# Optimization experiments

Measured on AMD Instinct MI355X. Metric: run time of the kernel, lower is better.

Reference implementation:

```python
import jax, jax.numpy as jnp
import numpy as np

B, N, CIN, COUT, MAXN, NF, MID = 8, 512, 64, 64, 16, 32, 16
M1 = [3, 32, 32, 1]
M2 = [CIN * COUT, 512, MID]
MR = [CIN * MID, 512, COUT]
BN_EPS = 1e-3  # keras BatchNormalization default epsilon


def mish(v):
    return v * jnp.tanh(jax.nn.softplus(v))


def bn(v, g, b):
    # training-mode batch norm over the row axis (keras BN in learning phase)
    mu = jnp.mean(v, axis=0, keepdims=True)
    var = jnp.var(v, axis=0, keepdims=True)
    return g * (v - mu) * jax.lax.rsqrt(var + BN_EPS) + b


def _mlp(v, layers):
    for W, b, g, be in layers:
        v = bn(mish(v @ W + b), g, be)
    return v


def setup_inputs() -> dict:
    key = jax.random.key(0)
    ks = jax.random.split(key, 16)
    inp = {
        'x': jax.random.normal(ks[0], (B, N, CIN), jnp.float32),
        'xyz': jax.random.normal(ks[1], (B, N, 3), jnp.float32),
        'framepoints': jax.random.normal(ks[2], (NF, 3), jnp.float32),
        'fpw': jax.random.normal(ks[3], (NF, CIN, COUT), jnp.float32) * 0.05,
    }
    ki = 4
    for name, dims in (('m1', M1), ('m2', M2), ('mr', MR)):
        for i in range(len(dims) - 1):
            inp[f'{name}_w{i}'] = jax.random.normal(ks[ki], (dims[i], dims[i + 1]), jnp.float32) / np.float32(np.sqrt(dims[i]))
            inp[f'{name}_b{i}'] = jnp.zeros((dims[i + 1],), jnp.float32)
            inp[f'{name}_g{i}'] = jnp.ones((dims[i + 1],), jnp.float32)
            inp[f'{name}_be{i}'] = jnp.zeros((dims[i + 1],), jnp.float32)
            ki += 1
    return inp


def reference(x, xyz, framepoints, fpw,
              m1_w0, m1_b0, m1_g0, m1_be0,
              m1_w1, m1_b1, m1_g1, m1_be1,
              m1_w2, m1_b2, m1_g2, m1_be2,
              m2_w0, m2_b0, m2_g0, m2_be0,
              m2_w1, m2_b1, m2_g1, m2_be1,
              mr_w0, mr_b0, mr_g0, mr_be0,
              mr_w1, mr_b1, mr_g1, mr_be1):
    Bc, Nc, cin = x.shape
    nf = framepoints.shape[0]
    cout = fpw.shape[2]
    mid = m2_w1.shape[1]

    # pairwise squared distances on FEATURES (as in the original), gram form
    sq = jnp.sum(x * x, axis=-1)  # [B,N]
    d = sq[:, :, None] + sq[:, None, :] - 2.0 * jnp.einsum('bnc,bmc->bnm', x, x)
    _, idx = jax.lax.top_k(-d, MAXN)  # [B,N,maxn] nearest (self first)

    bidx = jnp.arange(Bc)[:, None, None]
    xyz_sl = xyz[bidx, idx]  # [B,N,maxn,3]
    fur = x[bidx, idx]       # [B,N,maxn,cin]

    xyz_sl = xyz_sl.reshape(-1, MAXN, 3)
    rel = (xyz_sl - xyz_sl[:, :1, :]).reshape(-1, 3)  # [B*N*maxn, 3]

    # deterministic random rotation of frame points about the y axis
    ang = jax.random.uniform(jax.random.key(42), ()) * 2.0 * jnp.pi
    c = jnp.cos(ang); s = jnp.sin(ang)
    z = jnp.zeros_like(c); o = jnp.ones_like(c)
    R = jnp.stack([jnp.stack([c, z, s]), jnp.stack([z, o, z]), jnp.stack([-s, z, c])])
    fp = framepoints @ R  # [nf,3]

    sl = jnp.concatenate([rel, fp], axis=0)              # [M+nf, 3]
    diff = (sl[:, None, :] - fp[None, :, :]).reshape(-1, 3)  # [(M+nf)*nf, 3]

    h = _mlp(diff, [(m1_w0, m1_b0, m1_g0, m1_be0),
                    (m1_w1, m1_b1, m1_g1, m1_be1),
                    (m1_w2, m1_b2, m1_g2, m1_be2)])      # [(M+nf)*nf, 1]

    w = _mlp(fpw.reshape(nf, -1), [(m2_w0, m2_b0, m2_g0, m2_be0),
                                   (m2_w1, m2_b1, m2_g1, m2_be1)])  # [nf, mid]

    agg = jnp.sum(h.reshape(-1, nf, 1) * w[None], axis=1)  # [M+nf, mid]
    wmain = agg[:-nf].reshape(-1, MAXN, mid)               # [B*N, maxn, mid]

    f = jnp.einsum('kmc,kmd->kcd', fur.reshape(-1, MAXN, cin), wmain)
    f = f.reshape(-1, cin * mid)
    f = _mlp(f, [(mr_w0, mr_b0, mr_g0, mr_be0),
                 (mr_w1, mr_b1, mr_g1, mr_be1)])           # [B*N, cout]
    return f.reshape(Bc, Nc, cout)
```

## Files before the change

### kernel.cpp

```cpp
#include <hip/hip_runtime.h>
#include <math.h>

#define BB    8
#define NN    512
#define CIN   64
#define MAXN  16
#define NF    32
#define MID   16
#define BN_   4096
#define MSL   65536
#define MTOT  65568
#define RROWS 2098176
#define P2STR 40

typedef unsigned short ushort_t;
typedef __attribute__((ext_vector_type(8))) short bf16x8;
typedef __attribute__((ext_vector_type(4))) float f32x4;

__device__ __forceinline__ float mishf(float x){
  float t  = __expf(x);
  float u  = 1.0f + t;
  float u2 = u * u;
  float r  = x * (u2 - 1.0f) * __builtin_amdgcn_rcpf(u2 + 1.0f);
  return (x > 15.0f) ? x : r;
}

__device__ __forceinline__ ushort_t f2bf(float f){
  unsigned u = __float_as_uint(f);
  unsigned r = (u + 0x7FFFu + ((u >> 16) & 1u)) >> 16;
  return (ushort_t)r;
}

__device__ __forceinline__ unsigned cvt_pk_bf16(float lo, float hi){
  unsigned r;
  asm("v_cvt_pk_bf16_f32 %0, %1, %2" : "=v"(r) : "v"(lo), "v"(hi));
  return r;
}

__device__ __forceinline__ unsigned rotl32(unsigned v, unsigned s){
  return (v << s) | (v >> (32u - s));
}

__device__ __forceinline__ float jax_uniform42(){
  unsigned ks[3];
  ks[0] = 0u; ks[1] = 42u; ks[2] = 0x1BD11BDAu ^ 0u ^ 42u;
  const unsigned rot[8] = {13u,15u,26u,6u,17u,29u,16u,24u};
  unsigned x0 = ks[0];
  unsigned x1 = ks[1];
  #pragma unroll
  for (int blk = 0; blk < 5; ++blk){
    #pragma unroll
    for (int r = 0; r < 4; ++r){
      x0 += x1;
      x1 = rotl32(x1, rot[(blk & 1) * 4 + r]);
      x1 ^= x0;
    }
    x0 += ks[(blk + 1) % 3];
    x1 += ks[(blk + 2) % 3] + (unsigned)(blk + 1);
  }
  unsigned w = x0 ^ x1;
  return __uint_as_float((w >> 9) | 0x3f800000u) - 1.0f;
}

__global__ __launch_bounds__(256) void k_sq(const float* __restrict__ x, double* __restrict__ sqd){
  int r = blockIdx.x * 256 + threadIdx.x;
  const float4* p = (const float4*)(x + (size_t)r * 64);
  double a0 = 0.0, a1 = 0.0, a2 = 0.0, a3 = 0.0;
  #pragma unroll
  for (int k = 0; k < 16; k += 4){
    float4 v0 = p[k], v1 = p[k+1], v2 = p[k+2], v3 = p[k+3];
    a0 += (double)v0.x*v0.x + (double)v0.y*v0.y + (double)v0.z*v0.z + (double)v0.w*v0.w;
    a1 += (double)v1.x*v1.x + (double)v1.y*v1.y + (double)v1.z*v1.z + (double)v1.w*v1.w;
    a2 += (double)v2.x*v2.x + (double)v2.y*v2.y + (double)v2.z*v2.z + (double)v2.w*v2.w;
    a3 += (double)v3.x*v3.x + (double)v3.y*v3.y + (double)v3.z*v3.z + (double)v3.w*v3.w;
  }
  sqd[r] = (a0 + a1) + (a2 + a3);
}

__global__ __launch_bounds__(256) void k_topk(const float* __restrict__ x, const double* __restrict__ sqd,
                                              int* __restrict__ idxp){
  __shared__ float ct[128 * 65];
  __shared__ float xnl[4][64];
  int tid  = threadIdx.x;
  int lane = tid & 63;
  int wid  = tid >> 6;
  int g = blockIdx.x * 4 + wid;
  int b = g >> 9;
  const float* xb = x + (size_t)b * (NN * CIN);
  {
    int w = tid >> 6, c = tid & 63;
    int nq = (blockIdx.x * 4 + w) & 511;
    xnl[w][c] = xb[nq * 64 + c];
  }
  double sqn = sqd[g];

  double dst[8];
  #pragma unroll 1
  for (int tile = 0; tile < 4; ++tile){
    __syncthreads();
    #pragma unroll
    for (int u = 0; u < 8; ++u){
      int idx = u * 256 + tid;
      int row = idx >> 4, q = idx & 15;
      float4 v = *(const float4*)&xb[(size_t)(tile * 128 + row) * 64 + q * 4];
      float* d = &ct[row * 65 + q * 4];
      d[0] = v.x; d[1] = v.y; d[2] = v.z; d[3] = v.w;
    }
    __syncthreads();
    double a[2][4];
    #pragma unroll
    for (int s = 0; s < 2; ++s)
      #pragma unroll
      for (int i = 0; i < 4; ++i) a[s][i] = 0.0;
    #pragma unroll
    for (int k = 0; k < 16; ++k){
      float4 qv = *(const float4*)&xnl[wid][k * 4];
      double q0 = (double)qv.x, q1 = (double)qv.y, q2 = (double)qv.z, q3 = (double)qv.w;
      #pragma unroll
      for (int s = 0; s < 2; ++s){
        const float* rp = &ct[(lane + 64 * s) * 65 + k * 4];
        a[s][0] += q0 * (double)rp[0];
        a[s][1] += q1 * (double)rp[1];
        a[s][2] += q2 * (double)rp[2];
        a[s][3] += q3 * (double)rp[3];
      }
    }
    #pragma unroll
    for (int s = 0; s < 2; ++s){
      int m = tile * 128 + 64 * s + lane;
      dst[tile * 2 + s] = sqn + sqd[(b << 9) + m] - 2.0 * ((a[s][0] + a[s][1]) + (a[s][2] + a[s][3]));
    }
  }

  for (int it = 0; it < 16; ++it){
    double bd = 1.0e300; int bi = 0x7FFFFFFF;
    #pragma unroll
    for (int j = 0; j < 8; ++j){
      int m = ((j >> 1) << 7) + ((j & 1) << 6) + lane;
      if (dst[j] < bd){ bd = dst[j]; bi = m; }
    }
    #pragma unroll
    for (int off = 1; off < 64; off <<= 1){
      double od = __shfl_xor(bd, off);
      int    oi = __shfl_xor(bi, off);
      if (od < bd || (od == bd && oi < bi)){ bd = od; bi = oi; }
    }
    if (lane == 0) idxp[g * 16 + it] = bi;
    if (lane == (bi & 63)){
      int slot = ((bi >> 7) << 1) | ((bi >> 6) & 1);
      #pragma unroll
      for (int j = 0; j < 8; ++j) if (j == slot) dst[j] = 1.0e300;
    }
  }
}

__global__ __launch_bounds__(256) void k_prep(const float* __restrict__ xyz,
                                              const float* __restrict__ fpts,
                                              const int* __restrict__ idxp,
                                              const float* __restrict__ w0, const float* __restrict__ b0,
                                              float* __restrict__ sib, float* __restrict__ fjt){
  __shared__ float w0l[96], b0l[32];
  int tid = threadIdx.x;
  if (tid < 96) w0l[tid] = w0[tid];
  else if (tid < 128) b0l[tid - 96] = b0[tid - 96];
  __syncthreads();
  int i = blockIdx.x * 256 + tid;
  if (i >= MTOT) return;
  float vx, vy, vz;
  if (i < MSL){
    int bn = i >> 4, m = i & 15, b = bn >> 9;
    int i0 = idxp[bn * 16];
    int im = idxp[bn * 16 + m];
    const float* xz = xyz + (size_t)b * (NN * 3);
    vx = xz[im * 3 + 0] - xz[i0 * 3 + 0];
    vy = xz[im * 3 + 1] - xz[i0 * 3 + 1];
    vz = xz[im * 3 + 2] - xz[i0 * 3 + 2];
  } else {
    int j = i - MSL;
    float u   = jax_uniform42();
    float ang = (u * 2.0f) * 3.14159274f;
    float c = cosf(ang), s = sinf(ang);
    float fx = fpts[j * 3 + 0], fy = fpts[j * 3 + 1], fz = fpts[j * 3 + 2];
    vx = fx * c - fz * s;
    vy = fy;
    vz = fx * s + fz * c;
  }
  float si[32];
  #pragma unroll
  for (int c = 0; c < 32; ++c)
    si[c] = vx * w0l[c] + vy * w0l[32 + c] + vz * w0l[64 + c];
  float* dst = sib + (size_t)i * 32;
  #pragma unroll
  for (int cq = 0; cq < 8; ++cq){
    float4 o = make_float4(si[cq*4+0] + b0l[cq*4+0], si[cq*4+1] + b0l[cq*4+1],
                           si[cq*4+2] + b0l[cq*4+2], si[cq*4+3] + b0l[cq*4+3]);
    *(float4*)&dst[cq*4] = o;
  }
  if (i >= MSL){
    int j = i - MSL;
    #pragma unroll
    for (int c = 0; c < 32; ++c) fjt[c * 32 + j] = si[c];
  }
}

__global__ __launch_bounds__(256) void k_m1_p1(const float* __restrict__ sib, const float* __restrict__ fjt,
                                               float* __restrict__ s0g, float* __restrict__ q0g,
                                               ushort_t* __restrict__ a0g){
  __shared__ float fjlt[32 * 33];
  __shared__ float red[16][32], redq[16][32];
  int tid = threadIdx.x;
  for (int t = tid; t < 1024; t += 256) fjlt[(t & 31) * 33 + (t >> 5)] = fjt[t];
  __syncthreads();
  int c2 = (tid & 15) * 2, s = tid >> 4;
  float as0 = 0.0f, aq0 = 0.0f, as1 = 0.0f, aq1 = 0.0f;
  int base = blockIdx.x * 1024;
  #pragma unroll 4
  for (int t = 0; t < 64; ++t){
    int r = base + t * 16 + s;
    int i = r >> 5, j = r & 31;
    float2 v = *(const float2*)&sib[(size_t)i * 32 + c2];
    float2 f = *(const float2*)&fjlt[j * 33 + c2];
    float m0 = mishf(v.x - f.x);
    float m1 = mishf(v.y - f.y);
    as0 += m0; aq0 += m0 * m0;
    as1 += m1; aq1 += m1 * m1;
    if (a0g) *(unsigned*)&a0g[(size_t)r * 32 + c2] = cvt_pk_bf16(m0, m1);
  }
  red[s][c2] = as0;  red[s][c2 + 1] = as1;
  redq[s][c2] = aq0; redq[s][c2 + 1] = aq1;
  __syncthreads();
  if (tid < 32){
    float ts = 0.0f, tq = 0.0f;
    #pragma unroll
    for (int ss = 0; ss < 16; ++ss){ ts += red[ss][tid]; tq += redq[ss][tid]; }
    int bank = (blockIdx.x & 15) * 32 + tid;
    atomicAdd(&s0g[bank], ts);
    atomicAdd(&q0g[bank], tq);
  }
}

__global__ __launch_bounds__(256) void k_m1_setup(const float* __restrict__ w1g, const float* __restrict__ b1g,
                                                  const float* __restrict__ g0, const float* __restrict__ be0,
                                                  const float* __restrict__ s0g, const float* __restrict__ q0g,
                                                  float* __restrict__ biasXg, ushort_t* __restrict__ wtsb){
  __shared__ float A0l[32], C0l[32];
  int tid = threadIdx.x;
  if (tid < 32){
    float s = 0.0f, q = 0.0f;
    #pragma unroll
    for (int b = 0; b < 16; ++b){ s += s0g[b * 32 + tid]; q += q0g[b * 32 + tid]; }
    const float invR = 1.0f / (float)RROWS;
    float mu = s * invR, var = q * invR - mu * mu;
    float A = g0[tid] * rsqrtf(var + 1e-3f);
    A0l[tid] = A; C0l[tid] = be0[tid] - mu * A;
  }
  __syncthreads();
  if (tid < 32){
    float acc = b1g[tid];
    #pragma unroll
    for (int k = 0; k < 32; ++k) acc += C0l[k] * w1g[k * 32 + tid];
    biasXg[tid] = acc;
  }
  for (int t = tid; t < 1024; t += 256){
    int k = t >> 5, c = t & 31;
    wtsb[c * 32 + k] = f2bf(w1g[t] * A0l[k]);
  }
}

__global__ __launch_bounds__(256, 8) void k_m1_p2f(const ushort_t* __restrict__ a0g,
                                                   const ushort_t* __restrict__ wtsb,
                                                   const float* __restrict__ biasXg,
                                                   float* __restrict__ s1g, float* __restrict__ q1g,
                                                   ushort_t* __restrict__ a1b){
  __shared__ float satm[32], qatm[32];
  int tid = threadIdx.x;
  if (tid < 32){ satm[tid] = 0.0f; qatm[tid] = 0.0f; }
  __syncthreads();
  int lane = tid & 63, w = tid >> 6;
  int ln15 = lane & 15, quad = lane >> 4;
  bf16x8 bfr0 = *(const bf16x8*)&wtsb[ln15 * 32 + quad * 8];
  bf16x8 bfr1 = *(const bf16x8*)&wtsb[(16 + ln15) * 32 + quad * 8];
  f32x4 zero = {0.0f, 0.0f, 0.0f, 0.0f};
  f32x4 acc[4][2];
  size_t rowt = (size_t)blockIdx.x * 256;
  #pragma unroll
  for (int i2 = 0; i2 < 4; ++i2){
    int row = (w * 4 + i2) * 16 + ln15;
    bf16x8 af = *(const bf16x8*)&a0g[(rowt + row) * 32 + quad * 8];
    acc[i2][0] = __builtin_amdgcn_mfma_f32_16x16x32_bf16(af, bfr0, zero, 0, 0, 0);
    acc[i2][1] = __builtin_amdgcn_mfma_f32_16x16x32_bf16(af, bfr1, zero, 0, 0, 0);
  }
  float cs[2] = {0.0f, 0.0f}, cq2[2] = {0.0f, 0.0f};
  size_t rowbase = rowt + w * 64 + quad * 4;
  #pragma unroll
  for (int nt = 0; nt < 2; ++nt){
    int col = nt * 16 + ln15;
    float bx = biasXg[col];
    size_t colbase = (size_t)col * RROWS;
    #pragma unroll
    for (int i2 = 0; i2 < 4; ++i2){
      f32x4 a = acc[i2][nt];
      float m0 = mishf(a[0] + bx);
      float m1 = mishf(a[1] + bx);
      float m2 = mishf(a[2] + bx);
      float m3 = mishf(a[3] + bx);
      cs[nt]  += m0 + m1 + m2 + m3;
      cq2[nt] += m0*m0 + m1*m1 + m2*m2 + m3*m3;
      uint2 pk;
      pk.x = cvt_pk_bf16(m0, m1);
      pk.y = cvt_pk_bf16(m2, m3);
      *(uint2*)&a1b[colbase + rowbase + (size_t)i2 * 16] = pk;
    }
  }
  #pragma unroll
  for (int nt = 0; nt < 2; ++nt){
    float v = cs[nt], u = cq2[nt];
    v += __shfl_xor(v, 16); u += __shfl_xor(u, 16);
    v += __shfl_xor(v, 32); u += __shfl_xor(u, 32);
    if (lane < 16){
      atomicAdd(&satm[nt * 16 + ln15], v);
      atomicAdd(&qatm[nt * 16 + ln15], u);
    }
  }
  __syncthreads();
  if (tid < 32){
    int bank = (blockIdx.x & 15) * 32 + tid;
    atomicAdd(&s1g[bank], satm[tid]);
    atomicAdd(&q1g[bank], qatm[tid]);
  }
}

__global__ __launch_bounds__(256, 6) void k_m1_p2(const float* __restrict__ sib, const float* __restrict__ fjt,
                                               const float* __restrict__ w1g, const float* __restrict__ b1g,
                                               const float* __restrict__ g0, const float* __restrict__ be0,
                                               const float* __restrict__ s0g, const float* __restrict__ q0g,
                                               float* __restrict__ s1g, float* __restrict__ q1g,
                                               ushort_t* __restrict__ a1b){
  __shared__ __align__(16) ushort_t a0s[256 * P2STR];
  __shared__ __align__(16) float uni[1024];
  __shared__ float A0l[32], C0l[32], biasX[32], satm[32], qatm[32];
  ushort_t* wts = (ushort_t*)uni;
  int tid = threadIdx.x;
  for (int t = tid; t < 1024; t += 256) uni[t] = fjt[t];
  if (tid < 32){
    float s = 0.0f, q = 0.0f;
    #pragma unroll
    for (int b = 0; b < 16; ++b){ s += s0g[b * 32 + tid]; q += q0g[b * 32 + tid]; }
    const float invR = 1.0f / (float)RROWS;
    float mu = s * invR, var = q * invR - mu * mu;
    float A = g0[tid] * rsqrtf(var + 1e-3f);
    A0l[tid] = A; C0l[tid] = be0[tid] - mu * A;
    satm[tid] = 0.0f; qatm[tid] = 0.0f;
  }
  __syncthreads();
  {
    int r = blockIdx.x * 256 + tid;
    int i = r >> 5, j = r & 31;
    const float* sr = sib + (size_t)i * 32;
    ushort_t* dst = &a0s[tid * P2STR];
    #pragma unroll
    for (int cq = 0; cq < 4; ++cq){
      float4 sa = *(const float4*)&sr[cq * 8];
      float4 sb = *(const float4*)&sr[cq * 8 + 4];
      float m0 = mishf(sa.x - uni[(cq*8+0)*32 + j]);
      float m1 = mishf(sa.y - uni[(cq*8+1)*32 + j]);
      float m2 = mishf(sa.z - uni[(cq*8+2)*32 + j]);
      float m3 = mishf(sa.w - uni[(cq*8+3)*32 + j]);
      float m4 = mishf(sb.x - uni[(cq*8+4)*32 + j]);
      float m5 = mishf(sb.y - uni[(cq*8+5)*32 + j]);
      float m6 = mishf(sb.z - uni[(cq*8+6)*32 + j]);
      float m7 = mishf(sb.w - uni[(cq*8+7)*32 + j]);
      uint4 pk;
      pk.x = cvt_pk_bf16(m0, m1);
      pk.y = cvt_pk_bf16(m2, m3);
      pk.z = cvt_pk_bf16(m4, m5);
      pk.w = cvt_pk_bf16(m6, m7);
      *(uint4*)&dst[cq * 8] = pk;
    }
  }
  if (tid < 32){
    float acc = b1g[tid];
    #pragma unroll
    for (int k = 0; k < 32; ++k) acc += C0l[k] * w1g[k * 32 + tid];
    biasX[tid] = acc;
  }
  __syncthreads();
  for (int t = tid; t < 1024; t += 256){
    int k = t >> 5, c = t & 31;
    wts[c * P2STR + k] = f2bf(w1g[t] * A0l[k]);
  }
  __syncthreads();
  int lane = tid & 63, w = tid >> 6;
  int ln15 = lane & 15, quad = lane >> 4;
  f32x4 zero = {0.0f, 0.0f, 0.0f, 0.0f};
  bf16x8 bfr0 = *(bf16x8*)&wts[(ln15) * P2STR + quad * 8];
  bf16x8 bfr1 = *(bf16x8*)&wts[(16 + ln15) * P2STR + quad * 8];
  f32x4 acc[4][2];
  #pragma unroll
  for (int i2 = 0; i2 < 4; ++i2){
    int row = (w * 4 + i2) * 16 + ln15;
    bf16x8 af = *(bf16x8*)&a0s[row * P2STR + quad * 8];
    acc[i2][0] = __builtin_amdgcn_mfma_f32_16x16x32_bf16(af, bfr0, zero, 0, 0, 0);
    acc[i2][1] = __builtin_amdgcn_mfma_f32_16x16x32_bf16(af, bfr1, zero, 0, 0, 0);
  }
  float cs[2] = {0.0f, 0.0f}, cq2[2] = {0.0f, 0.0f};
  size_t rowbase = (size_t)blockIdx.x * 256 + w * 64 + quad * 4;
  #pragma unroll
  for (int nt = 0; nt < 2; ++nt){
    int col = nt * 16 + ln15;
    float bx = biasX[col];
    size_t colbase = (size_t)col * RROWS;
    #pragma unroll
    for (int i2 = 0; i2 < 4; ++i2){
      f32x4 a = acc[i2][nt];
      float m0 = mishf(a[0] + bx);
      float m1 = mishf(a[1] + bx);
      float m2 = mishf(a[2] + bx);
      float m3 = mishf(a[3] + bx);
      cs[nt]  += m0 + m1 + m2 + m3;
      cq2[nt] += m0*m0 + m1*m1 + m2*m2 + m3*m3;
      if (a1b){
        uint2 pk;
        pk.x = cvt_pk_bf16(m0, m1);
        pk.y = cvt_pk_bf16(m2, m3);
        *(uint2*)&a1b[colbase + rowbase + (size_t)i2 * 16] = pk;
      }
    }
  }
  #pragma unroll
  for (int nt = 0; nt < 2; ++nt){
    float v = cs[nt], u = cq2[nt];
    v += __shfl_xor(v, 16); u += __shfl_xor(u, 16);
    v += __shfl_xor(v, 32); u += __shfl_xor(u, 32);
    if (lane < 16){
      atomicAdd(&satm[nt * 16 + ln15], v);
      atomicAdd(&qatm[nt * 16 + ln15], u);
    }
  }
  __syncthreads();
  if (tid < 32){
    int bank = (blockIdx.x & 15) * 32 + tid;
    atomicAdd(&s1g[bank], satm[tid]);
    atomicAdd(&q1g[bank], qatm[tid]);
  }
}

__global__ __launch_bounds__(256) void k_m1_p3s(const ushort_t* __restrict__ a1b,
                                                const float* __restrict__ w2g, const float* __restrict__ b2g,
                                                const float* __restrict__ g1, const float* __restrict__ be1,
                                                const float* __restrict__ s1g, const float* __restrict__ q1g,
                                                float* __restrict__ act2, float* __restrict__ s2g, float* __restrict__ q2g){
  __shared__ float vvl[32], C1l[32], cb2l[1], r2s[4], r2q[4];
  int tid = threadIdx.x;
  if (tid < 32){
    float s = 0.0f, q = 0.0f;
    #pragma unroll
    for (int b = 0; b < 16; ++b){ s += s1g[b * 32 + tid]; q += q1g[b * 32 + tid]; }
    const float invR = 1.0f / (float)RROWS;
    float mu = s * invR, var = q * invR - mu * mu;
    float A = g1[tid] * rsqrtf(var + 1e-3f);
    C1l[tid] = be1[tid] - mu * A;
    vvl[tid] = A * w2g[tid];
  }
  __syncthreads();
  if (tid == 0){
    float a = b2g[0];
    #pragma unroll
    for (int k = 0; k < 32; ++k) a += C1l[k] * w2g[k];
    cb2l[0] = a;
  }
  __syncthreads();
  size_t r0 = (size_t)blockIdx.x * 2048 + (size_t)tid * 8;
  float ss = 0.0f, qq = 0.0f;
  if (r0 < (size_t)RROWS){
    float pre[8];
    #pragma unroll
    for (int j = 0; j < 8; ++j) pre[j] = 0.0f;
    #pragma unroll 8
    for (int c = 0; c < 32; ++c){
      uint4 u = *(const uint4*)&a1b[(size_t)c * RROWS + r0];
      float vv = vvl[c];
      pre[0] += __uint_as_float(u.x << 16) * vv;
      pre[1] += __uint_as_float(u.x & 0xFFFF0000u) * vv;
      pre[2] += __uint_as_float(u.y << 16) * vv;
      pre[3] += __uint_as_float(u.y & 0xFFFF0000u) * vv;
      pre[4] += __uint_as_float(u.z << 16) * vv;
      pre[5] += __uint_as_float(u.z & 0xFFFF0000u) * vv;
      pre[6] += __uint_as_float(u.w << 16) * vv;
      pre[7] += __uint_as_float(u.w & 0xFFFF0000u) * vv;
    }
    float cb2 = cb2l[0];
    float a2[8];
    #pragma unroll
    for (int j = 0; j < 8; ++j){
      a2[j] = mishf(pre[j] + cb2);
      ss += a2[j]; qq += a2[j] * a2[j];
    }
    *(float4*)&act2[r0]     = make_float4(a2[0], a2[1], a2[2], a2[3]);
    *(float4*)&act2[r0 + 4] = make_float4(a2[4], a2[5], a2[6], a2[7]);
  }
  #pragma unroll
  for (int off = 1; off < 64; off <<= 1){ ss += __shfl_xor(ss, off); qq += __shfl_xor(qq, off); }
  int lane = tid & 63, wid = tid >> 6;
  if (lane == 0){ r2s[wid] = ss; r2q[wid] = qq; }
  __syncthreads();
  if (tid == 0){
    atomicAdd(&s2g[blockIdx.x & 15], r2s[0] + r2s[1] + r2s[2] + r2s[3]);
    atomicAdd(&q2g[blockIdx.x & 15], r2q[0] + r2q[1] + r2q[2] + r2q[3]);
  }
}

__global__ __launch_bounds__(256, 3) void k_m1_p3f(const float* __restrict__ sib, const float* __restrict__ fjt,
                                               const float* __restrict__ w1g, const float* __restrict__ b1g,
                                               const float* __restrict__ g0, const float* __restrict__ be0,
                                               const float* __restrict__ g1, const float* __restrict__ be1,
                                               const float* __restrict__ w2g, const float* __restrict__ b2g,
                                               const float* __restrict__ s0g, const float* __restrict__ q0g,
                                               const float* __restrict__ s1g, const float* __restrict__ q1g,
                                               float* __restrict__ act2, float* __restrict__ s2g, float* __restrict__ q2g){
  __shared__ float fjl[1024];
  __shared__ float w1s[1024];
  __shared__ float A0l[32], C0l[32], A1l[32], C1l[32], biasX[32], vvl[32];
  __shared__ float a0t[32 * 256];
  __shared__ float cb2l[1];
  __shared__ float r2s[4], r2q[4];
  int tid = threadIdx.x;
  const float invR = 1.0f / (float)RROWS;
  for (int t = tid; t < 1024; t += 256) fjl[t] = fjt[t];
  if (tid < 32){
    float s = 0.0f, q = 0.0f;
    #pragma unroll
    for (int b = 0; b < 16; ++b){ s += s0g[b * 32 + tid]; q += q0g[b * 32 + tid]; }
    float mu = s * invR, var = q * invR - mu * mu;
    float A = g0[tid] * rsqrtf(var + 1e-3f);
    A0l[tid] = A; C0l[tid] = be0[tid] - mu * A;
  } else if (tid < 64){
    int c = tid - 32;
    float s = 0.0f, q = 0.0f;
    #pragma unroll
    for (int b = 0; b < 16; ++b){ s += s1g[b * 32 + c]; q += q1g[b * 32 + c]; }
    float mu = s * invR, var = q * invR - mu * mu;
    float A = g1[c] * rsqrtf(var + 1e-3f);
    A1l[c] = A; C1l[c] = be1[c] - mu * A;
  }
  __syncthreads();
  for (int t = tid; t < 1024; t += 256) w1s[t] = w1g[t] * A0l[t >> 5];
  if (tid < 32){
    float acc = b1g[tid];
    #pragma unroll
    for (int k = 0; k < 32; ++k) acc += C0l[k] * w1g[k * 32 + tid];
    biasX[tid] = acc;
  } else if (tid < 96 && tid >= 64){
    int c = tid - 64;
    vvl[c] = A1l[c] * w2g[c];
  } else if (tid == 96){
    float acc = b2g[0];
    #pragma unroll
    for (int k = 0; k < 32; ++k) acc += C1l[k] * w2g[k];
    cb2l[0] = acc;
  }
  {
    int r = blockIdx.x * 256 + tid;
    int i = r >> 5, j = r & 31;
    const float* sr = sib + (size_t)i * 32;
    #pragma unroll
    for (int cq = 0; cq < 8; ++cq){
      float4 sv = *(const float4*)&sr[cq * 4];
      a0t[(cq*4+0)*256 + tid] = mishf(sv.x - fjl[(cq*4+0)*32 + j]);
      a0t[(cq*4+1)*256 + tid] = mishf(sv.y - fjl[(cq*4+1)*32 + j]);
      a0t[(cq*4+2)*256 + tid] = mishf(sv.z - fjl[(cq*4+2)*32 + j]);
      a0t[(cq*4+3)*256 + tid] = mishf(sv.w - fjl[(cq*4+3)*32 + j]);
    }
  }
  __syncthreads();
  int cg = tid & 7, rg = tid >> 3;
  float acc[8][4];
  #pragma unroll
  for (int i2 = 0; i2 < 8; ++i2)
    #pragma unroll
    for (int j2 = 0; j2 < 4; ++j2) acc[i2][j2] = 0.0f;
  #pragma unroll 4
  for (int k = 0; k < 32; ++k){
    float4 w  = *(const float4*)&w1s[k * 32 + cg * 4];
    float4 aA = *(const float4*)&a0t[k * 256 + rg * 8];
    float4 aB = *(const float4*)&a0t[k * 256 + rg * 8 + 4];
    float ar[8] = {aA.x, aA.y, aA.z, aA.w, aB.x, aB.y, aB.z, aB.w};
    float wc[4] = {w.x, w.y, w.z, w.w};
    #pragma unroll
    for (int i2 = 0; i2 < 8; ++i2)
      #pragma unroll
      for (int j2 = 0; j2 < 4; ++j2) acc[i2][j2] += ar[i2] * wc[j2];
  }
  float cb2 = cb2l[0];
  float ss = 0.0f, qq = 0.0f;
  #pragma unroll
  for (int rr = 0; rr < 8; ++rr){
    float part = 0.0f;
    #pragma unroll
    for (int cc = 0; cc < 4; ++cc){
      float m = mishf(acc[rr][cc] + biasX[cg * 4 + cc]);
      part += m * vvl[cg * 4 + cc];
    }
    part += __shfl_xor(part, 1);
    part += __shfl_xor(part, 2);
    part += __shfl_xor(part, 4);
    float a2 = mishf(part + cb2);
    if (cg == 0){
      act2[(size_t)blockIdx.x * 256 + rg * 8 + rr] = a2;
      ss += a2; qq += a2 * a2;
    }
  }
  #pragma unroll
  for (int off = 1; off < 64; off <<= 1){ ss += __shfl_xor(ss, off); qq += __shfl_xor(qq, off); }
  int lane = tid & 63, wid = tid >> 6;
  if (lane == 0){ r2s[wid] = ss; r2q[wid] = qq; }
  __syncthreads();
  if (tid == 0){
    atomicAdd(&s2g[blockIdx.x & 15], r2s[0] + r2s[1] + r2s[2] + r2s[3]);
    atomicAdd(&q2g[blockIdx.x & 15], r2q[0] + r2q[1] + r2q[2] + r2q[3]);
  }
}

__global__ __launch_bounds__(512) void k_wmlp1(const float* __restrict__ fpw, const float* __restrict__ W0,
                                               float* __restrict__ wact0){
  int f = blockIdx.x, kc = blockIdx.y, c = threadIdx.x;
  const float* row = fpw + (size_t)f * 4096 + kc * 512;
  const float* wp  = W0 + (size_t)(kc * 512) * 512 + c;
  float acc = 0.0f;
  #pragma unroll 8
  for (int k = 0; k < 512; ++k) acc += row[k] * wp[(size_t)k * 512];
  atomicAdd(&wact0[f * 512 + c], acc);
}

__global__ __launch_bounds__(512) void k_wmlp2(const float* __restrict__ wact0, const float* __restrict__ b0,
                                               const float* __restrict__ W1,
                                               const float* __restrict__ b1,
                                               const float* __restrict__ g0, const float* __restrict__ be0,
                                               const float* __restrict__ g1, const float* __restrict__ be1,
                                               float* __restrict__ wfin){
  __shared__ float wl[32 * 512];
  __shared__ float o2l[512], A1l[16], C1l[16];
  int t = threadIdx.x;
  {
    float b0t = b0[t];
    float v[32]; float sum = 0.0f, sq = 0.0f;
    #pragma unroll
    for (int r = 0; r < 32; ++r){
      v[r] = mishf(wact0[r * 512 + t] + b0t);
      sum += v[r]; sq += v[r] * v[r];
    }
    float mu  = sum * (1.0f / 32.0f);
    float var = sq * (1.0f / 32.0f) - mu * mu;
    float A = g0[t] * rsqrtf(var + 1e-3f);
    float C = be0[t] - mu * A;
    #pragma unroll
    for (int r = 0; r < 32; ++r) wl[r * 512 + t] = v[r] * A + C;
  }
  __syncthreads();
  {
    int r = t >> 4, c2 = t & 15;
    float pre = b1[c2];
    for (int k = 0; k < 512; ++k) pre += wl[r * 512 + k] * W1[k * 16 + c2];
    o2l[t] = mishf(pre);
  }
  __syncthreads();
  if (t < 16){
    float sum = 0.0f, sq = 0.0f;
    #pragma unroll
    for (int r = 0; r < 32; ++r){ float v = o2l[r * 16 + t]; sum += v; sq += v * v; }
    float mu  = sum * (1.0f / 32.0f);
    float var = sq * (1.0f / 32.0f) - mu * mu;
    float A = g1[t] * rsqrtf(var + 1e-3f);
    A1l[t] = A; C1l[t] = be1[t] - mu * A;
  }
  __syncthreads();
  wfin[t] = o2l[t] * A1l[t & 15] + C1l[t & 15];
}

__global__ __launch_bounds__(256) void k_agg(const float* __restrict__ act2, const float* __restrict__ wfin,
                                             const float* __restrict__ x, const int* __restrict__ idxp,
                                             const float* __restrict__ s2, const float* __restrict__ q2,
                                             const float* __restrict__ g2, const float* __restrict__ be2,
                                             ushort_t* __restrict__ fb16){
  __shared__ float hl[512], wfl[512], wm[256], furl[1024], AC[2];
  int t = threadIdx.x;
  int k = blockIdx.x;
  if (t == 0){
    const float invR = 1.0f / (float)RROWS;
    float ssum = 0.0f, qsum = 0.0f;
    #pragma unroll
    for (int b = 0; b < 16; ++b){ ssum += s2[b]; qsum += q2[b]; }
    float mu  = ssum * invR;
    float var = qsum * invR - mu * mu;
    float A = g2[0] * rsqrtf(var + 1e-3f);
    AC[0] = A; AC[1] = be2[0] - mu * A;
  }
  wfl[t] = wfin[t]; wfl[t + 256] = wfin[t + 256];
  __syncthreads();
  float A2 = AC[0], C2 = AC[1];
  hl[t]       = act2[(size_t)k * 512 + t]       * A2 + C2;
  hl[t + 256] = act2[(size_t)k * 512 + 256 + t] * A2 + C2;
  __syncthreads();
  {
    int m = t >> 4, d = t & 15;
    float acc = 0.0f;
    #pragma unroll
    for (int j = 0; j < 32; ++j) acc += hl[m * 32 + j] * wfl[j * 16 + d];
    wm[t] = acc;
  }
  int b = k >> 9;
  const float* xb = x + (size_t)b * (NN * CIN);
  {
    int c = t & 63;
    #pragma unroll
    for (int it = 0; it < 4; ++it){
      int m = it * 4 + (t >> 6);
      int im = idxp[k * 16 + m];
      furl[m * 64 + c] = xb[im * 64 + c];
    }
  }
  __syncthreads();
  {
    int d = t & 15, c0 = t >> 4;
    #pragma unroll
    for (int q = 0; q < 4; ++q){
      int c = c0 + 16 * q;
      float acc = 0.0f;
      #pragma unroll
      for (int m = 0; m < 16; ++m) acc += furl[m * 64 + c] * wm[m * 16 + d];
      fb16[(size_t)k * 1024 + t + 256 * q] = f2bf(acc);
    }
  }
}

__global__ __launch_bounds__(256) void k_w2bf(const float* __restrict__ W, ushort_t* __restrict__ Wb){
  int id = blockIdx.x * 256 + threadIdx.x;
  int n  = id >> 7;
  int k8 = (id & 127) * 8;
  float v[8];
  #pragma unroll
  for (int j = 0; j < 8; ++j) v[j] = W[(size_t)(k8 + j) * 512 + n];
  uint4 p;
  p.x = cvt_pk_bf16(v[0], v[1]);
  p.y = cvt_pk_bf16(v[2], v[3]);
  p.z = cvt_pk_bf16(v[4], v[5]);
  p.w = cvt_pk_bf16(v[6], v[7]);
  *(uint4*)&Wb[(size_t)n * 1024 + k8] = p;
}

__global__ __launch_bounds__(256, 8) void k_mr1(const ushort_t* __restrict__ F16, const ushort_t* __restrict__ Wb,
                                             const float* __restrict__ bias, float* __restrict__ out,
                                             float* __restrict__ s3, float* __restrict__ q3){
  __shared__ float csum[64], csq[64];
  int tid = threadIdx.x;
  int m0 = blockIdx.y * 64, n0 = blockIdx.x * 64;
  int lane = tid & 63, w = tid >> 6;
  int ln15 = lane & 15, quad = lane >> 4;
  if (tid < 64){ csum[tid] = 0.0f; csq[tid] = 0.0f; }
  __syncthreads();
  f32x4 acc[4];
  #pragma unroll
  for (int n = 0; n < 4; ++n){ acc[n][0] = 0.0f; acc[n][1] = 0.0f; acc[n][2] = 0.0f; acc[n][3] = 0.0f; }
  const ushort_t* Arow = &F16[(size_t)(m0 + w * 16 + ln15) * 1024 + quad * 8];
  const ushort_t* B0 = &Wb[(size_t)(n0 +  0 + ln15) * 1024 + quad * 8];
  const ushort_t* B1 = &Wb[(size_t)(n0 + 16 + ln15) * 1024 + quad * 8];
  const ushort_t* B2 = &Wb[(size_t)(n0 + 32 + ln15) * 1024 + quad * 8];
  const ushort_t* B3 = &Wb[(size_t)(n0 + 48 + ln15) * 1024 + quad * 8];
  #pragma unroll 4
  for (int k0 = 0; k0 < 1024; k0 += 32){
    bf16x8 af = *(const bf16x8*)&Arow[k0];
    bf16x8 b0 = *(const bf16x8*)&B0[k0];
    bf16x8 b1 = *(const bf16x8*)&B1[k0];
    bf16x8 b2 = *(const bf16x8*)&B2[k0];
    bf16x8 b3 = *(const bf16x8*)&B3[k0];
    acc[0] = __builtin_amdgcn_mfma_f32_16x16x32_bf16(af, b0, acc[0], 0, 0, 0);
    acc[1] = __builtin_amdgcn_mfma_f32_16x16x32_bf16(af, b1, acc[1], 0, 0, 0);
    acc[2] = __builtin_amdgcn_mfma_f32_16x16x32_bf16(af, b2, acc[2], 0, 0, 0);
    acc[3] = __builtin_amdgcn_mfma_f32_16x16x32_bf16(af, b3, acc[3], 0, 0, 0);
  }
  #pragma unroll
  for (int n = 0; n < 4; ++n){
    int col = n0 + n * 16 + ln15;
    float bv = bias[col];
    f32x4 a = acc[n];
    float s = 0.0f, q = 0.0f;
    #pragma unroll
    for (int r = 0; r < 4; ++r){
      float v = mishf(a[r] + bv);
      int row = m0 + w * 16 + quad * 4 + r;
      out[(size_t)row * 512 + col] = v;
      s += v; q += v * v;
    }
    s += __shfl_xor(s, 16); q += __shfl_xor(q, 16);
    s += __shfl_xor(s, 32); q += __shfl_xor(q, 32);
    if (quad == 0){
      atomicAdd(&csum[n * 16 + ln15], s);
      atomicAdd(&csq[n * 16 + ln15], q);
    }
  }
  __syncthreads();
  if (tid < 64){
    atomicAdd(&s3[n0 + tid], csum[tid]);
    atomicAdd(&q3[n0 + tid], csq[tid]);
  }
}

__global__ __launch_bounds__(256) void k_mr2(const float* __restrict__ Ain, const float* __restrict__ W,
                                             const float* __restrict__ bias,
                                             const float* __restrict__ s3, const float* __restrict__ q3,
                                             const float* __restrict__ g0, const float* __restrict__ be0,
                                             float* __restrict__ out, float* __restrict__ s4, float* __restrict__ q4){
  __shared__ float As2[16][68];
  __shared__ float Bs2[16][68];
  __shared__ float A3l[512], C3l[512];
  __shared__ float csum[64], csq[64];
  int tid = threadIdx.x;
  for (int kk = tid; kk < 512; kk += 256){
    const float invR = 1.0f / 4096.0f;
    float mu  = s3[kk] * invR;
    float var = q3[kk] * invR - mu * mu;
    float A = g0[kk] * rsqrtf(var + 1e-3f);
    A3l[kk] = A; C3l[kk] = be0[kk] - mu * A;
  }
  if (tid < 64){ csum[tid] = 0.0f; csq[tid] = 0.0f; }
  __syncthreads();
  int m0 = blockIdx.x * 64;
  int tx = tid & 15, ty = tid >> 4;
  float acc[4][4];
  #pragma unroll
  for (int i = 0; i < 4; ++i)
    #pragma unroll
    for (int j = 0; j < 4; ++j) acc[i][j] = 0.0f;
  int lmm = tid >> 2, lkq = (tid & 3) * 4;
  int lkk = tid >> 4, lnq = (tid & 15) * 4;
  float4 av = *(const float4*)&Ain[(size_t)(m0 + lmm) * 512 + lkq];
  float4 bv = *(const float4*)&W[(size_t)lkk * 64 + lnq];
  for (int k0 = 0; k0 < 512; k0 += 16){
    As2[lkq + 0][lmm] = av.x * A3l[k0 + lkq + 0] + C3l[k0 + lkq + 0];
    As2[lkq + 1][lmm] = av.y * A3l[k0 + lkq + 1] + C3l[k0 + lkq + 1];
    As2[lkq + 2][lmm] = av.z * A3l[k0 + lkq + 2] + C3l[k0 + lkq + 2];
    As2[lkq + 3][lmm] = av.w * A3l[k0 + lkq + 3] + C3l[k0 + lkq + 3];
    *(float4*)&Bs2[lkk][lnq] = bv;
    __syncthreads();
    if (k0 + 16 < 512){
      av = *(const float4*)&Ain[(size_t)(m0 + lmm) * 512 + (k0 + 16) + lkq];
      bv = *(const float4*)&W[(size_t)((k0 + 16) + lkk) * 64 + lnq];
    }
    #pragma unroll
    for (int kk = 0; kk < 16; ++kk){
      float4 a4 = *(const float4*)&As2[kk][ty * 4];
      float4 b4 = *(const float4*)&Bs2[kk][tx * 4];
      float a[4] = {a4.x, a4.y, a4.z, a4.w};
      float bb[4] = {b4.x, b4.y, b4.z, b4.w};
      #pragma unroll
      for (int i = 0; i < 4; ++i)
        #pragma unroll
        for (int j = 0; j < 4; ++j) acc[i][j] += a[i] * bb[j];
    }
    __syncthreads();
  }
  float4 bq = *(const float4*)&bias[tx * 4];
  float bvs[4] = {bq.x, bq.y, bq.z, bq.w};
  float cs[4] = {0,0,0,0}, cq[4] = {0,0,0,0};
  #pragma unroll
  for (int i = 0; i < 4; ++i){
    float v[4];
    #pragma unroll
    for (int j = 0; j < 4; ++j){
      v[j] = mishf(acc[i][j] + bvs[j]);
      cs[j] += v[j]; cq[j] += v[j] * v[j];
    }
    float4 o = make_float4(v[0], v[1], v[2], v[3]);
    *(float4*)&out[(size_t)(m0 + ty * 4 + i) * 64 + tx * 4] = o;
  }
  #pragma unroll
  for (int j = 0; j < 4; ++j){
    float v = cs[j], w = cq[j];
    v += __shfl_xor(v, 16); w += __shfl_xor(w, 16);
    v += __shfl_xor(v, 32); w += __shfl_xor(w, 32);
    if ((tid & 63) < 16){
      atomicAdd(&csum[tx * 4 + j], v);
      atomicAdd(&csq[tx * 4 + j], w);
    }
  }
  __syncthreads();
  if (tid < 64){
    atomicAdd(&s4[tid], csum[tid]);
    atomicAdd(&q4[tid], csq[tid]);
  }
}

__global__ __launch_bounds__(256) void k_out(const float* __restrict__ pre,
                                             const float* __restrict__ s4, const float* __restrict__ q4,
                                             const float* __restrict__ g1, const float* __restrict__ be1,
                                             float* __restrict__ outp){
  int e = blockIdx.x * 256 + threadIdx.x;
  int c = e & 63;
  const float invR = 1.0f / 4096.0f;
  float mu  = s4[c] * invR;
  float var = q4[c] * invR - mu * mu;
  float A = g1[c] * rsqrtf(var + 1e-3f);
  outp[e] = pre[e] * A + (be1[c] - mu * A);
}

extern "C" void kernel_launch(void* const* d_in, const int* in_sizes, int n_in,
                              void* d_out, int out_size, void* d_ws, size_t ws_size,
                              hipStream_t stream){
  (void)in_sizes; (void)n_in; (void)out_size;
  const float* x    = (const float*)d_in[0];
  const float* xyz  = (const float*)d_in[1];
  const float* fpts = (const float*)d_in[2];
  const float* fpw  = (const float*)d_in[3];
  const float* m1w0 = (const float*)d_in[4];
  const float* m1b0 = (const float*)d_in[5];
  const float* m1g0 = (const float*)d_in[6];
  const float* m1be0= (const float*)d_in[7];
  const float* m1w1 = (const float*)d_in[8];
  const float* m1b1 = (const float*)d_in[9];
  const float* m1g1 = (const float*)d_in[10];
  const float* m1be1= (const float*)d_in[11];
  const float* m1w2 = (const float*)d_in[12];
  const float* m1b2 = (const float*)d_in[13];
  const float* m1g2 = (const float*)d_in[14];
  const float* m1be2= (const float*)d_in[15];
  const float* m2w0 = (const float*)d_in[16];
  const float* m2b0 = (const float*)d_in[17];
  const float* m2g0 = (const float*)d_in[18];
  const float* m2be0= (const float*)d_in[19];
  const float* m2w1 = (const float*)d_in[20];
  const float* m2b1 = (const float*)d_in[21];
  const float* m2g1 = (const float*)d_in[22];
  const float* m2be1= (const float*)d_in[23];
  const float* mrw0 = (const float*)d_in[24];
  const float* mrb0 = (const float*)d_in[25];
  const float* mrg0 = (const float*)d_in[26];
  const float* mrbe0= (const float*)d_in[27];
  const float* mrw1 = (const float*)d_in[28];
  const float* mrb1 = (const float*)d_in[29];
  const float* mrg1 = (const float*)d_in[30];
  const float* mrbe1= (const float*)d_in[31];

  float* wsf = (float*)d_ws;
  float* s0 = wsf + 0;     float* q0 = wsf + 512;
  float* s1 = wsf + 1024;  float* q1 = wsf + 1536;
  float* s2 = wsf + 2048;  float* q2 = wsf + 2064;
  float* s3 = wsf + 2080;  float* q3 = wsf + 2592;
  float* s4 = wsf + 3104;  float* q4 = wsf + 3168;
  int*   idxp = (int*)(wsf + 4096);
  double* sqd = (double*)(wsf + 69632);
  float* biasXg = wsf + 77824;
  ushort_t* wtsb = (ushort_t*)(wsf + 77856);
  float* wact0= wsf + 332032;
  float* wfin = wsf + 348416;
  float* act2 = wsf + 348928;
  float* fbuf = wsf + 2447104;
  float* sib  = fbuf;
  float* fjt  = fbuf + 2098176;
  ushort_t* fb16 = (ushort_t*)fbuf;
  ushort_t* wb16 = (ushort_t*)(fbuf + 2099200);
  float* mact = wsf + 6641408;
  float* mact2= wsf + 8738560;

  size_t need1 = 9000704ULL * 4 + (size_t)RROWS * 32 * 2;
  size_t need2 = need1 + (size_t)RROWS * 32 * 2;
  bool fast = (ws_size >= need1);
  bool t2   = (ws_size >= need2);
  ushort_t* a1b = fast ? (ushort_t*)(wsf + 9000704) : nullptr;
  ushort_t* a0g = t2   ? (ushort_t*)(wsf + 9000704 + 33570816) : nullptr;

  hipMemsetAsync(d_ws, 0, 4096 * sizeof(float), stream);
  hipMemsetAsync(wact0, 0, 16384 * sizeof(float), stream);

  k_w2bf<<<256, 256, 0, stream>>>(mrw0, wb16);
  k_sq<<<16, 256, 0, stream>>>(x, sqd);
  k_topk<<<1024, 256, 0, stream>>>(x, sqd, idxp);
  k_prep<<<257, 256, 0, stream>>>(xyz, fpts, idxp, m1w0, m1b0, sib, fjt);
  k_m1_p1<<<2049, 256, 0, stream>>>(sib, fjt, s0, q0, a0g);
  if (t2){
    k_m1_setup<<<1, 256, 0, stream>>>(m1w1, m1b1, m1g0, m1be0, s0, q0, biasXg, wtsb);
    k_m1_p2f<<<8196, 256, 0, stream>>>(a0g, wtsb, biasXg, s1, q1, a1b);
  } else {
    k_m1_p2<<<8196, 256, 0, stream>>>(sib, fjt, m1w1, m1b1, m1g0, m1be0, s0, q0, s1, q1, a1b);
  }
  if (fast){
    k_m1_p3s<<<1025, 256, 0, stream>>>(a1b, m1w2, m1b2, m1g1, m1be1, s1, q1, act2, s2, q2);
  } else {
    k_m1_p3f<<<8196, 256, 0, stream>>>(sib, fjt, m1w1, m1b1, m1g0, m1be0, m1g1, m1be1,
                                       m1w2, m1b2, s0, q0, s1, q1, act2, s2, q2);
  }
  k_wmlp1<<<dim3(32, 8), 512, 0, stream>>>(fpw, m2w0, wact0);
  k_wmlp2<<<1, 512, 0, stream>>>(wact0, m2b0, m2w1, m2b1, m2g0, m2be0, m2g1, m2be1, wfin);
  k_agg<<<4096, 256, 0, stream>>>(act2, wfin, x, idxp, s2, q2, m1g2, m1be2, fb16);
  k_mr1<<<dim3(8, 64), 256, 0, stream>>>(fb16, wb16, mrb0, mact, s3, q3);
  k_mr2<<<64, 256, 0, stream>>>(mact, mrw1, mrb1, s3, q3, mrg0, mrbe0, mact2, s4, q4);
  k_out<<<1024, 256, 0, stream>>>(mact2, s4, q4, mrg1, mrbe1, (float*)d_out);
}
```

Baseline: 446.3 us.

## Reuse one row-major bf16 buffer for layer-1 and layer-2 MLP activations in place

The second MLP layer now writes its bf16 activations back into the same row-major buffer that held its input, instead of into a separate column-major buffer. The third-layer kernel is rewritten to read 32 contiguous bf16 values per row and reduce them. This halves the workspace needed for the fast path, so the MFMA path runs whenever the single buffer fits. In-place writes are 2-byte scattered stores per lane, which may coalesce worse than the previous packed column stores, and they rely on each block only overwriting rows it has already read.

```diff
diff --git a/kernel.cpp b/kernel.cpp
--- a/kernel.cpp
+++ b/kernel.cpp
@@ -267,11 +267,10 @@
   }
 }
 
-__global__ __launch_bounds__(256, 8) void k_m1_p2f(const ushort_t* __restrict__ a0g,
+__global__ __launch_bounds__(256, 8) void k_m1_p2f(ushort_t* __restrict__ ab,
                                                    const ushort_t* __restrict__ wtsb,
                                                    const float* __restrict__ biasXg,
-                                                   float* __restrict__ s1g, float* __restrict__ q1g,
-                                                   ushort_t* __restrict__ a1b){
+                                                   float* __restrict__ s1g, float* __restrict__ q1g){
   __shared__ float satm[32], qatm[32];
   int tid = threadIdx.x;
   if (tid < 32){ satm[tid] = 0.0f; qatm[tid] = 0.0f; }
@@ -286,17 +285,15 @@
   #pragma unroll
   for (int i2 = 0; i2 < 4; ++i2){
     int row = (w * 4 + i2) * 16 + ln15;
-    bf16x8 af = *(const bf16x8*)&a0g[(rowt + row) * 32 + quad * 8];
+    bf16x8 af = *(const bf16x8*)&ab[(rowt + row) * 32 + quad * 8];
     acc[i2][0] = __builtin_amdgcn_mfma_f32_16x16x32_bf16(af, bfr0, zero, 0, 0, 0);
     acc[i2][1] = __builtin_amdgcn_mfma_f32_16x16x32_bf16(af, bfr1, zero, 0, 0, 0);
   }
   float cs[2] = {0.0f, 0.0f}, cq2[2] = {0.0f, 0.0f};
-  size_t rowbase = rowt + w * 64 + quad * 4;
   #pragma unroll
   for (int nt = 0; nt < 2; ++nt){
     int col = nt * 16 + ln15;
     float bx = biasXg[col];
-    size_t colbase = (size_t)col * RROWS;
     #pragma unroll
     for (int i2 = 0; i2 < 4; ++i2){
       f32x4 a = acc[i2][nt];
@@ -306,10 +303,13 @@
       float m3 = mishf(a[3] + bx);
       cs[nt]  += m0 + m1 + m2 + m3;
       cq2[nt] += m0*m0 + m1*m1 + m2*m2 + m3*m3;
-      uint2 pk;
-      pk.x = cvt_pk_bf16(m0, m1);
-      pk.y = cvt_pk_bf16(m2, m3);
-      *(uint2*)&a1b[colbase + rowbase + (size_t)i2 * 16] = pk;
+      unsigned p01 = cvt_pk_bf16(m0, m1);
+      unsigned p23 = cvt_pk_bf16(m2, m3);
+      size_t rb = rowt + (size_t)w * 64 + i2 * 16 + quad * 4;
+      ab[(rb + 0) * 32 + col] = (ushort_t)p01;
+      ab[(rb + 1) * 32 + col] = (ushort_t)(p01 >> 16);
+      ab[(rb + 2) * 32 + col] = (ushort_t)p23;
+      ab[(rb + 3) * 32 + col] = (ushort_t)(p23 >> 16);
     }
   }
   #pragma unroll
@@ -445,7 +445,7 @@
   }
 }
 
-__global__ __launch_bounds__(256) void k_m1_p3s(const ushort_t* __restrict__ a1b,
+__global__ __launch_bounds__(256) void k_m1_p3r(const ushort_t* __restrict__ ab,
                                                 const float* __restrict__ w2g, const float* __restrict__ b2g,
                                                 const float* __restrict__ g1, const float* __restrict__ be1,
                                                 const float* __restrict__ s1g, const float* __restrict__ q1g,
@@ -470,34 +470,25 @@
     cb2l[0] = a;
   }
   __syncthreads();
-  size_t r0 = (size_t)blockIdx.x * 2048 + (size_t)tid * 8;
+  float cb2 = cb2l[0];
+  size_t base = (size_t)blockIdx.x * 1024 + tid;
   float ss = 0.0f, qq = 0.0f;
-  if (r0 < (size_t)RROWS){
-    float pre[8];
-    #pragma unroll
-    for (int j = 0; j < 8; ++j) pre[j] = 0.0f;
-    #pragma unroll 8
-    for (int c = 0; c < 32; ++c){
-      uint4 u = *(const uint4*)&a1b[(size_t)c * RROWS + r0];
-      float vv = vvl[c];
-      pre[0] += __uint_as_float(u.x << 16) * vv;
-      pre[1] += __uint_as_float(u.x & 0xFFFF0000u) * vv;
-      pre[2] += __uint_as_float(u.y << 16) * vv;
-      pre[3] += __uint_as_float(u.y & 0xFFFF0000u) * vv;
-      pre[4] += __uint_as_float(u.z << 16) * vv;
-      pre[5] += __uint_as_float(u.z & 0xFFFF0000u) * vv;
-      pre[6] += __uint_as_float(u.w << 16) * vv;
-      pre[7] += __uint_as_float(u.w & 0xFFFF0000u) * vv;
-    }
-    float cb2 = cb2l[0];
-    float a2[8];
-    #pragma unroll
-    for (int j = 0; j < 8; ++j){
-      a2[j] = mishf(pre[j] + cb2);
-      ss += a2[j]; qq += a2[j] * a2[j];
-    }
-    *(float4*)&act2[r0]     = make_float4(a2[0], a2[1], a2[2], a2[3]);
-    *(float4*)&act2[r0 + 4] = make_float4(a2[4], a2[5], a2[6], a2[7]);
+  #pragma unroll
+  for (int k4 = 0; k4 < 4; ++k4){
+    size_t r = base + (size_t)k4 * 256;
+    const uint4* p = (const uint4*)&ab[r * 32];
+    uint4 ua = p[0], ub = p[1], uc = p[2], ud = p[3];
+    unsigned us[16] = {ua.x, ua.y, ua.z, ua.w, ub.x, ub.y, ub.z, ub.w,
+                       uc.x, uc.y, uc.z, uc.w, ud.x, ud.y, ud.z, ud.w};
+    float p0 = 0.0f, p1 = 0.0f;
+    #pragma unroll
+    for (int q = 0; q < 16; ++q){
+      p0 += __uint_as_float(us[q] << 16) * vvl[2 * q];
+      p1 += __uint_as_float(us[q] & 0xFFFF0000u) * vvl[2 * q + 1];
+    }
+    float a2 = mishf(p0 + p1 + cb2);
+    act2[r] = a2;
+    ss += a2; qq += a2 * a2;
   }
   #pragma unroll
   for (int off = 1; off < 64; off <<= 1){ ss += __shfl_xor(ss, off); qq += __shfl_xor(qq, off); }
@@ -962,11 +953,8 @@
   float* mact2= wsf + 8738560;
 
   size_t need1 = 9000704ULL * 4 + (size_t)RROWS * 32 * 2;
-  size_t need2 = need1 + (size_t)RROWS * 32 * 2;
   bool fast = (ws_size >= need1);
-  bool t2   = (ws_size >= need2);
-  ushort_t* a1b = fast ? (ushort_t*)(wsf + 9000704) : nullptr;
-  ushort_t* a0g = t2   ? (ushort_t*)(wsf + 9000704 + 33570816) : nullptr;
+  ushort_t* ab = fast ? (ushort_t*)(wsf + 9000704) : nullptr;
 
   hipMemsetAsync(d_ws, 0, 4096 * sizeof(float), stream);
   hipMemsetAsync(wact0, 0, 16384 * sizeof(float), stream);
@@ -975,16 +963,13 @@
   k_sq<<<16, 256, 0, stream>>>(x, sqd);
   k_topk<<<1024, 256, 0, stream>>>(x, sqd, idxp);
   k_prep<<<257, 256, 0, stream>>>(xyz, fpts, idxp, m1w0, m1b0, sib, fjt);
-  k_m1_p1<<<2049, 256, 0, stream>>>(sib, fjt, s0, q0, a0g);
-  if (t2){
+  k_m1_p1<<<2049, 256, 0, stream>>>(sib, fjt, s0, q0, ab);
+  if (fast){
     k_m1_setup<<<1, 256, 0, stream>>>(m1w1, m1b1, m1g0, m1be0, s0, q0, biasXg, wtsb);
-    k_m1_p2f<<<8196, 256, 0, stream>>>(a0g, wtsb, biasXg, s1, q1, a1b);
+    k_m1_p2f<<<8196, 256, 0, stream>>>(ab, wtsb, biasXg, s1, q1);
+    k_m1_p3r<<<2049, 256, 0, stream>>>(ab, m1w2, m1b2, m1g1, m1be1, s1, q1, act2, s2, q2);
   } else {
-    k_m1_p2<<<8196, 256, 0, stream>>>(sib, fjt, m1w1, m1b1, m1g0, m1be0, s0, q0, s1, q1, a1b);
-  }
-  if (fast){
-    k_m1_p3s<<<1025, 256, 0, stream>>>(a1b, m1w2, m1b2, m1g1, m1be1, s1, q1, act2, s2, q2);
-  } else {
+    k_m1_p2<<<8196, 256, 0, stream>>>(sib, fjt, m1w1, m1b1, m1g0, m1be0, s0, q0, s1, q1, nullptr);
     k_m1_p3f<<<8196, 256, 0, stream>>>(sib, fjt, m1w1, m1b1, m1g0, m1be0, m1g1, m1be1,
                                        m1w2, m1b2, s0, q0, s1, q1, act2, s2, q2);
   }
```

Measured after the change: 451.2 us. Within noise of the previous version (+1.1%).
